# Optimization experiments

Measured on AMD Instinct MI355X. Metric: run time of the kernel, lower is better.

The kernel has to match this reference:

```python
import jax, jax.numpy as jnp
import numpy as np


def setup_inputs() -> dict:
    key = jax.random.key(0)
    ks = jax.random.split(key, 20)
    B, T, E, U, D, O = 64, 2048, 256, 256, 256, 32000
    s = lambda k, shp, fan: (jax.random.normal(k, shp, jnp.float32) * (1.0 / np.sqrt(fan)))
    return {
        'inputs': jax.random.normal(ks[0], (B, D), jnp.float32),
        'stm': jax.random.normal(ks[1], (B, U), jnp.float32),
        'x_seq': jax.random.normal(ks[2], (B, T, E), jnp.float32),
        'V_a': s(ks[3], (U + E,), U + E),
        'W_a': s(ks[4], (U + E, U + E), U + E),
        'W_r': s(ks[5], (D, U), D), 'U_r': s(ks[6], (U, U), U), 'C_r': s(ks[7], (E, U), E), 'b_r': jnp.zeros((U,), jnp.float32),
        'W_z': s(ks[8], (D, U), D), 'U_z': s(ks[9], (U, U), U), 'C_z': s(ks[10], (E, U), E), 'b_z': jnp.zeros((U,), jnp.float32),
        'W_p': s(ks[11], (D, U), D), 'U_p': s(ks[12], (U, U), U), 'C_p': s(ks[13], (E, U), E), 'b_p': jnp.zeros((U,), jnp.float32),
        'W_o': s(ks[14], (D, O), D), 'U_o': s(ks[15], (U, O), U), 'C_o': s(ks[16], (E, O), E), 'b_o': jnp.zeros((O,), jnp.float32),
    }


def reference(inputs, stm, x_seq, V_a, W_a,
              W_r, U_r, C_r, b_r,
              W_z, U_z, C_z, b_z,
              W_p, U_p, C_p, b_p,
              W_o, U_o, C_o, b_o):
    B, T, E = x_seq.shape
    U = stm.shape[-1]
    # Bahdanau additive attention: concat repeated state with encoder seq
    _stm = jnp.broadcast_to(stm[:, None, :], (B, T, U))          # [B,T,U]
    cat = jnp.concatenate([_stm, x_seq], axis=-1)                 # [B,T,U+E]
    et = jnp.einsum('btc,c->bt', jnp.tanh(jnp.einsum('btc,cd->btd', cat, W_a)), V_a)
    at = jax.nn.softmax(et, axis=1)                               # exp / sum over T
    context = jnp.einsum('bt,bte->be', at, x_seq)                 # [B,E]
    # GRU-style gates conditioned on input, previous state, and context
    rt = jax.nn.sigmoid(inputs @ W_r + stm @ U_r + context @ C_r + b_r)
    zt = jax.nn.sigmoid(inputs @ W_z + stm @ U_z + context @ C_z + b_z)
    s_tp = jnp.tanh(inputs @ W_p + (rt * stm) @ U_p + context @ C_p + b_p)
    st = (1.0 - zt) * stm + zt * s_tp                             # new state [B,U]
    output = jax.nn.softmax(inputs @ W_o + stm @ U_o + context @ C_o + b_o, axis=-1)  # [B,O]
    return output, st
```

## Files before the change

### kernel.cpp

```cpp
#include <hip/hip_runtime.h>
#include <hip/hip_bf16.h>

#define B_ 64
#define T_ 2048
#define E_ 256
#define U_ 256
#define O_ 32000
#define UE_ 512

typedef __attribute__((ext_vector_type(8))) short bf16x8;
typedef __attribute__((ext_vector_type(4))) float f32x4;

__device__ __forceinline__ unsigned short f2bf(float f){
  __hip_bfloat16 h = __float2bfloat16(f);
  return __builtin_bit_cast(unsigned short, h);
}
__device__ __forceinline__ unsigned pk2bf(float a, float b){
  return (unsigned)f2bf(a) | ((unsigned)f2bf(b) << 16);
}
__device__ __forceinline__ bf16x8 pack8(const float* v0, const float* v1){
  float4 x = *(const float4*)v0;
  float4 y = *(const float4*)v1;
  uint4 pk;
  pk.x = pk2bf(x.x, x.y); pk.y = pk2bf(x.z, x.w);
  pk.z = pk2bf(y.x, y.y); pk.w = pk2bf(y.z, y.w);
  return __builtin_bit_cast(bf16x8, pk);
}
__device__ __forceinline__ float ftanh(float x){
  float e = __expf(2.0f*x);
  return 1.0f - 2.0f/(e + 1.0f);
}
__device__ __forceinline__ float fsig(float x){
  return 1.0f/(1.0f + __expf(-x));
}

__global__ __launch_bounds__(256)
void prep_kernel(const float* __restrict__ Wa, const float* __restrict__ stm,
                 unsigned short* __restrict__ bpack, float* __restrict__ sp){
  if (blockIdx.x < 64){
    int idx = blockIdx.x*256 + threadIdx.x;
    int n = idx & 511;
    int ktg = idx >> 9;
    int erow = ktg * 8;
    unsigned short o[8];
#pragma unroll
    for (int i = 0; i < 8; ++i)
      o[i] = f2bf(Wa[(256 + erow + i)*512 + n]);
    uint4 v;
    v.x = (unsigned)o[0] | ((unsigned)o[1] << 16);
    v.y = (unsigned)o[2] | ((unsigned)o[3] << 16);
    v.z = (unsigned)o[4] | ((unsigned)o[5] << 16);
    v.w = (unsigned)o[6] | ((unsigned)o[7] << 16);
    ((uint4*)bpack)[idx] = v;
  } else {
    int tid = threadIdx.x;
    int w = tid >> 6, l = tid & 63, c = l & 15, g = l >> 4;
    int n0 = (blockIdx.x - 64)*64 + w*16;
    f32x4 zero = {0.f,0.f,0.f,0.f};
    f32x4 acc[4];
#pragma unroll
    for (int mt = 0; mt < 4; ++mt) acc[mt] = zero;
#pragma unroll
    for (int ks = 0; ks < 8; ++ks){
      int kg = ks*32 + 8*g;
      bf16x8 a[4];
#pragma unroll
      for (int mt = 0; mt < 4; ++mt){
        const float* ap = stm + (mt*16 + c)*256 + kg;
        a[mt] = pack8(ap, ap + 4);
      }
      const float* bpt = Wa + (size_t)kg*512 + n0 + c;
      float bv[8];
#pragma unroll
      for (int i = 0; i < 8; ++i) bv[i] = bpt[(size_t)i*512];
      uint4 pk;
      pk.x = pk2bf(bv[0], bv[1]); pk.y = pk2bf(bv[2], bv[3]);
      pk.z = pk2bf(bv[4], bv[5]); pk.w = pk2bf(bv[6], bv[7]);
      bf16x8 bfr = __builtin_bit_cast(bf16x8, pk);
#pragma unroll
      for (int mt = 0; mt < 4; ++mt)
        acc[mt] = __builtin_amdgcn_mfma_f32_16x16x32_bf16(a[mt], bfr, acc[mt], 0, 0, 0);
    }
#pragma unroll
    for (int mt = 0; mt < 4; ++mt)
#pragma unroll
      for (int r = 0; r < 4; ++r){
        int m = mt*16 + 4*g + r;
        sp[m*512 + n0 + c] = acc[mt][r];
      }
  }
}

__global__ __launch_bounds__(512, 4)
void et_flash_kernel(const float* __restrict__ xseq, const unsigned short* __restrict__ bpack,
                     const float* __restrict__ va, const float* __restrict__ sp,
                     float* __restrict__ msbuf, float* __restrict__ uctxp){
  __shared__ __align__(16) uint4 sA4[2048];
  __shared__ float sVa[512];
  __shared__ float sSp[512];
  __shared__ float sEt[8][64];
  __shared__ float sE[64];
  int tid = threadIdx.x;
  int w = tid >> 6, l = tid & 63, c = l & 15, g = l >> 4;
  int m0 = blockIdx.x * 64;
  int b  = m0 >> 11;

  const float4* x4 = (const float4*)xseq + (size_t)m0 * 64;
  uint2* sA2 = (uint2*)sA4;
#pragma unroll
  for (int i = 0; i < 8; ++i){
    int p = i*512 + tid;
    int row = p >> 6, kq = p & 63;
    float4 v = x4[row*64 + kq];
    uint2 u;
    u.x = pk2bf(v.x, v.y);
    u.y = pk2bf(v.z, v.w);
    int s = ((row>>4)*8 + (kq>>3))*64 + ((kq>>1)&3)*16 + (row&15);
    sA2[(s ^ ((s>>4)&7))*2 + (kq&1)] = u;
  }
  sVa[tid] = va[tid];
  sSp[tid] = sp[b*512 + tid];
  __syncthreads();

  f32x4 zero = {0.f, 0.f, 0.f, 0.f};
  f32x4 acc[4][4];
#pragma unroll
  for (int mt = 0; mt < 4; ++mt)
#pragma unroll
    for (int tc = 0; tc < 4; ++tc) acc[mt][tc] = zero;

  const bf16x8* bp = (const bf16x8*)bpack;
#pragma unroll
  for (int ks = 0; ks < 8; ++ks){
    bf16x8 aw[4], bx[4];
    int bbase = (ks*4 + g)*512 + w*64 + c;
#pragma unroll
    for (int mt = 0; mt < 4; ++mt)
      aw[mt] = bp[bbase + mt*16];
#pragma unroll
    for (int tc = 0; tc < 4; ++tc){
      int idx = (tc*8 + ks)*64 + l;
      bx[tc] = *(const bf16x8*)&sA4[idx ^ ((idx>>4)&7)];
    }
    __builtin_amdgcn_s_setprio(1);
#pragma unroll
    for (int mt = 0; mt < 4; ++mt)
#pragma unroll
      for (int tc = 0; tc < 4; ++tc)
        acc[mt][tc] = __builtin_amdgcn_mfma_f32_16x16x32_bf16(aw[mt], bx[tc], acc[mt][tc], 0, 0, 0);
    __builtin_amdgcn_s_setprio(0);
  }

  float p[4] = {0.f, 0.f, 0.f, 0.f};
#pragma unroll
  for (int mt = 0; mt < 4; ++mt){
    int nb = w*64 + mt*16 + 4*g;
    float4 vav = *(const float4*)&sVa[nb];
    float4 spv = *(const float4*)&sSp[nb];
#pragma unroll
    for (int tc = 0; tc < 4; ++tc){
#pragma unroll
      for (int r = 0; r < 4; ++r){
        float vv = acc[mt][tc][r] + ((const float*)&spv)[r];
        p[tc] += ((const float*)&vav)[r] * ftanh(vv);
      }
    }
  }
#pragma unroll
  for (int tc = 0; tc < 4; ++tc){
    p[tc] += __shfl_xor(p[tc], 16, 64);
    p[tc] += __shfl_xor(p[tc], 32, 64);
  }
  if (l < 16){
#pragma unroll
    for (int tc = 0; tc < 4; ++tc)
      sEt[w][tc*16 + c] = p[tc];
  }
  __syncthreads();

  if (tid < 64){
    float e = 0.f;
#pragma unroll
    for (int ww = 0; ww < 8; ++ww) e += sEt[ww][tid];
    float m = e;
#pragma unroll
    for (int off = 1; off < 64; off <<= 1) m = fmaxf(m, __shfl_xor(m, off, 64));
    float ex = __expf(e - m);
    float s = ex;
#pragma unroll
    for (int off = 1; off < 64; off <<= 1) s += __shfl_xor(s, off, 64);
    sE[tid] = ex;
    if (tid == 0){
      msbuf[blockIdx.x*2]     = m;
      msbuf[blockIdx.x*2 + 1] = s;
    }
  }
  __syncthreads();

  {
    int e = tid & 255, th = tid >> 8;
    int ks = e >> 5, gg = (e >> 3) & 3, ii = e & 7;
    const unsigned short* sU = (const unsigned short*)sA4;
    float a0 = 0.f;
#pragma unroll
    for (int tt = 0; tt < 32; ++tt){
      int t = th*32 + tt;
      int mt = t >> 4, cc = t & 15;
      int slt = (mt*8 + ks)*64 + gg*16 + cc;
      unsigned short hv = sU[(size_t)(slt ^ ((slt>>4)&7))*8 + ii];
      float xv = __builtin_bit_cast(float, ((unsigned)hv) << 16);
      a0 += sE[t] * xv;
    }
    uctxp[((size_t)blockIdx.x*2 + th)*256 + e] = a0;
  }
}

__global__ void ctx_x1_kernel(const float* __restrict__ msbuf, const float* __restrict__ uctxp,
                              const float* __restrict__ inputs, const float* __restrict__ stm,
                              unsigned short* __restrict__ X1bf){
  int b = blockIdx.x, e = threadIdx.x;
  float M = -INFINITY;
#pragma unroll 4
  for (int j = 0; j < 32; ++j) M = fmaxf(M, msbuf[(32*b + j)*2]);
  float S = 0.f;
  float acc = 0.f;
#pragma unroll 4
  for (int j = 0; j < 32; ++j){
    float wj = __expf(msbuf[(32*b + j)*2] - M);
    S += msbuf[(32*b + j)*2 + 1] * wj;
    size_t base = ((size_t)(32*b + j)*2)*256 + e;
    acc += (uctxp[base] + uctxp[base + 256]) * wj;
  }
  float ctx = acc / S;
  X1bf[b*768 + e]        = f2bf(inputs[b*256 + e]);
  X1bf[b*768 + 256 + e]  = f2bf(stm[b*256 + e]);
  X1bf[b*768 + 512 + e]  = f2bf(ctx);
}

__global__ __launch_bounds__(256)
void gates1_kernel(const unsigned short* __restrict__ X1bf, const float* __restrict__ stm,
                   const float* __restrict__ Wr, const float* __restrict__ Ur,
                   const float* __restrict__ Cr, const float* __restrict__ brr,
                   const float* __restrict__ Wz, const float* __restrict__ Uz,
                   const float* __restrict__ Cz, const float* __restrict__ bzz,
                   const float* __restrict__ Wp, const float* __restrict__ Cp,
                   const float* __restrict__ bpp,
                   float* __restrict__ rs, float* __restrict__ ztb, float* __restrict__ pic){
  int tid = threadIdx.x;
  int w = tid >> 6, l = tid & 63, c = l & 15, g = l >> 4;
  int n0 = blockIdx.x*64 + w*16;
  int gate = n0 >> 8;
  int col0 = n0 & 255;
  const float* W0; const float* W1; const float* W2; const float* bias;
  if (gate == 0){ W0 = Wr; W1 = Ur; W2 = Cr; bias = brr; }
  else if (gate == 1){ W0 = Wz; W1 = Uz; W2 = Cz; bias = bzz; }
  else { W0 = Wp; W1 = nullptr; W2 = Cp; bias = bpp; }

  f32x4 zero = {0.f,0.f,0.f,0.f};
  f32x4 acc[4];
#pragma unroll
  for (int mt = 0; mt < 4; ++mt) acc[mt] = zero;

#pragma unroll
  for (int ph = 0; ph < 3; ++ph){
    const float* src = (ph == 0) ? W0 : (ph == 1) ? W1 : W2;
    if (src == nullptr) continue;
#pragma unroll
    for (int ks = 0; ks < 8; ++ks){
      int kg = ks*32 + 8*g;
      bf16x8 a[4];
#pragma unroll
      for (int mt = 0; mt < 4; ++mt)
        a[mt] = *(const bf16x8*)&X1bf[(mt*16 + c)*768 + ph*256 + kg];
      const float* bpt = src + (size_t)kg*256 + col0 + c;
      float bv[8];
#pragma unroll
      for (int i = 0; i < 8; ++i) bv[i] = bpt[(size_t)i*256];
      uint4 pk;
      pk.x = pk2bf(bv[0], bv[1]); pk.y = pk2bf(bv[2], bv[3]);
      pk.z = pk2bf(bv[4], bv[5]); pk.w = pk2bf(bv[6], bv[7]);
      bf16x8 bfr = __builtin_bit_cast(bf16x8, pk);
#pragma unroll
      for (int mt = 0; mt < 4; ++mt)
        acc[mt] = __builtin_amdgcn_mfma_f32_16x16x32_bf16(a[mt], bfr, acc[mt], 0, 0, 0);
    }
  }

  int n = col0 + c;
  float bi = bias[n];
#pragma unroll
  for (int mt = 0; mt < 4; ++mt)
#pragma unroll
    for (int r = 0; r < 4; ++r){
      int m = mt*16 + 4*g + r;
      float pre = acc[mt][r] + bi;
      if (gate == 0)      rs[m*256 + n]  = fsig(pre) * stm[m*256 + n];
      else if (gate == 1) ztb[m*256 + n] = fsig(pre);
      else                pic[m*256 + n] = pre;
    }
}

__global__ __launch_bounds__(256)
void gates2_kernel(const float* __restrict__ rs, const float* __restrict__ Up,
                   const float* __restrict__ pic, const float* __restrict__ ztb,
                   const float* __restrict__ stm, float* __restrict__ stout){
  int tid = threadIdx.x;
  int w = tid >> 6, l = tid & 63, c = l & 15, g = l >> 4;
  int n0 = blockIdx.x*64 + w*16;
  f32x4 zero = {0.f,0.f,0.f,0.f};
  f32x4 acc[4];
#pragma unroll
  for (int mt = 0; mt < 4; ++mt) acc[mt] = zero;
#pragma unroll
  for (int ks = 0; ks < 8; ++ks){
    int kg = ks*32 + 8*g;
    bf16x8 a[4];
#pragma unroll
    for (int mt = 0; mt < 4; ++mt){
      const float* ap = rs + (mt*16 + c)*256 + kg;
      a[mt] = pack8(ap, ap + 4);
    }
    const float* bpt = Up + (size_t)kg*256 + n0 + c;
    float bv[8];
#pragma unroll
    for (int i = 0; i < 8; ++i) bv[i] = bpt[(size_t)i*256];
    uint4 pk;
    pk.x = pk2bf(bv[0], bv[1]); pk.y = pk2bf(bv[2], bv[3]);
    pk.z = pk2bf(bv[4], bv[5]); pk.w = pk2bf(bv[6], bv[7]);
    bf16x8 bfr = __builtin_bit_cast(bf16x8, pk);
#pragma unroll
    for (int mt = 0; mt < 4; ++mt)
      acc[mt] = __builtin_amdgcn_mfma_f32_16x16x32_bf16(a[mt], bfr, acc[mt], 0, 0, 0);
  }
#pragma unroll
  for (int mt = 0; mt < 4; ++mt)
#pragma unroll
    for (int r = 0; r < 4; ++r){
      int m = mt*16 + 4*g + r;
      int o = m*256 + n0 + c;
      float ap = pic[o] + acc[mt][r];
      float z = ztb[o];
      stout[o] = (1.f - z)*stm[o] + z*ftanh(ap);
    }
}

__global__ __launch_bounds__(512)
void logits_mfma_kernel(const unsigned short* __restrict__ X1bf,
                        const float* __restrict__ Wo, const float* __restrict__ Uo,
                        const float* __restrict__ Co, const float* __restrict__ boo,
                        float* __restrict__ outl, float* __restrict__ part2){
  __shared__ float sAcc[16][4][64];
  __shared__ float sMx[4][64];
  __shared__ float sSx[4][64];
  int tid = threadIdx.x;
  int w = tid >> 6, l = tid & 63, c = l & 15, g = l >> 4;
  int wc = w & 3;
  int kh = w >> 2;
  int n0 = blockIdx.x*64 + wc*16;
  f32x4 zero = {0.f,0.f,0.f,0.f};
  f32x4 acc[4];
#pragma unroll
  for (int mt = 0; mt < 4; ++mt) acc[mt] = zero;

#pragma unroll
  for (int ph = 0; ph < 3; ++ph){
    const float* src = (ph == 0) ? Wo : (ph == 1) ? Uo : Co;
#pragma unroll
    for (int kss = 0; kss < 4; ++kss){
      int ks = 2*kss + kh;
      int kg = ph*256 + ks*32 + 8*g;
      bf16x8 a[4];
#pragma unroll
      for (int mt = 0; mt < 4; ++mt)
        a[mt] = *(const bf16x8*)&X1bf[(mt*16 + c)*768 + kg];
      const float* bpt = src + (size_t)(ks*32 + 8*g)*32000 + n0 + c;
      float bv[8];
#pragma unroll
      for (int i = 0; i < 8; ++i) bv[i] = bpt[(size_t)i*32000];
      uint4 pk;
      pk.x = pk2bf(bv[0], bv[1]);
      pk.y = pk2bf(bv[2], bv[3]);
      pk.z = pk2bf(bv[4], bv[5]);
      pk.w = pk2bf(bv[6], bv[7]);
      bf16x8 bfr = __builtin_bit_cast(bf16x8, pk);
#pragma unroll
      for (int mt = 0; mt < 4; ++mt)
        acc[mt] = __builtin_amdgcn_mfma_f32_16x16x32_bf16(a[mt], bfr, acc[mt], 0, 0, 0);
    }
  }

  if (kh == 1){
#pragma unroll
    for (int mt = 0; mt < 4; ++mt)
#pragma unroll
      for (int r = 0; r < 4; ++r)
        sAcc[mt*4 + r][wc][l] = acc[mt][r];
  }
  __syncthreads();

  bool active = (kh == 0);
  float vv[4][4];
  if (active){
    float bias = boo[n0 + c];
#pragma unroll
    for (int mt = 0; mt < 4; ++mt)
#pragma unroll
      for (int r = 0; r < 4; ++r){
        int m = mt*16 + 4*g + r;
        vv[mt][r] = acc[mt][r] + sAcc[mt*4 + r][wc][l] + bias;
        outl[(size_t)m*32000 + n0 + c] = vv[mt][r];
      }
    float mx[4][4];
#pragma unroll
    for (int mt = 0; mt < 4; ++mt)
#pragma unroll
      for (int r = 0; r < 4; ++r) mx[mt][r] = vv[mt][r];
#pragma unroll
    for (int mask = 1; mask < 16; mask <<= 1)
#pragma unroll
      for (int mt = 0; mt < 4; ++mt)
#pragma unroll
        for (int r = 0; r < 4; ++r)
          mx[mt][r] = fmaxf(mx[mt][r], __shfl_xor(mx[mt][r], mask, 64));
    if (c == 0)
#pragma unroll
      for (int mt = 0; mt < 4; ++mt)
#pragma unroll
        for (int r = 0; r < 4; ++r)
          sMx[wc][mt*16 + 4*g + r] = mx[mt][r];
  }
  __syncthreads();
  if (active){
    float sx[4][4];
#pragma unroll
    for (int mt = 0; mt < 4; ++mt)
#pragma unroll
      for (int r = 0; r < 4; ++r){
        int row = mt*16 + 4*g + r;
        float M = fmaxf(fmaxf(sMx[0][row], sMx[1][row]), fmaxf(sMx[2][row], sMx[3][row]));
        sx[mt][r] = __expf(vv[mt][r] - M);
      }
#pragma unroll
    for (int mask = 1; mask < 16; mask <<= 1)
#pragma unroll
      for (int mt = 0; mt < 4; ++mt)
#pragma unroll
        for (int r = 0; r < 4; ++r)
          sx[mt][r] += __shfl_xor(sx[mt][r], mask, 64);
    if (c == 0)
#pragma unroll
      for (int mt = 0; mt < 4; ++mt)
#pragma unroll
        for (int r = 0; r < 4; ++r)
          sSx[wc][mt*16 + 4*g + r] = sx[mt][r];
  }
  __syncthreads();
  if (tid < 64){
    int row = tid;
    float M = fmaxf(fmaxf(sMx[0][row], sMx[1][row]), fmaxf(sMx[2][row], sMx[3][row]));
    float S = sSx[0][row] + sSx[1][row] + sSx[2][row] + sSx[3][row];
    part2[((size_t)blockIdx.x*64 + row)*2]     = M;
    part2[((size_t)blockIdx.x*64 + row)*2 + 1] = S;
  }
}

__global__ void sm_comb_kernel(const float* __restrict__ part2, float* __restrict__ fin){
  __shared__ float red[8];
  __shared__ float red2[8];
  int b = blockIdx.x;
  int tid = threadIdx.x;
  float M = -INFINITY, S = 0.f;
  if (tid < 500){
    M = part2[((size_t)tid*64 + b)*2];
    S = part2[((size_t)tid*64 + b)*2 + 1];
  }
  float m1 = M;
#pragma unroll
  for (int off = 1; off < 64; off <<= 1) m1 = fmaxf(m1, __shfl_xor(m1, off, 64));
  int wv = tid >> 6;
  if ((tid & 63) == 0) red[wv] = m1;
  __syncthreads();
  float Mg = red[0];
#pragma unroll
  for (int i = 1; i < 8; ++i) Mg = fmaxf(Mg, red[i]);
  float s1 = (tid < 500) ? S * __expf(M - Mg) : 0.f;
#pragma unroll
  for (int off = 1; off < 64; off <<= 1) s1 += __shfl_xor(s1, off, 64);
  if ((tid & 63) == 0) red2[wv] = s1;
  __syncthreads();
  if (tid == 0){
    float St = 0.f;
#pragma unroll
    for (int i = 0; i < 8; ++i) St += red2[i];
    fin[b*2] = Mg;
    fin[b*2 + 1] = St;
  }
}

__global__ void sm_norm_kernel(float* __restrict__ logits, const float* __restrict__ fin){
  int bid = blockIdx.x;
  int b = bid >> 3, ch = bid & 7;
  int base = b*32000 + ch*4000;
  int tid = threadIdx.x;
  float M = fin[2*b];
  float inv = 1.0f / fin[2*b + 1];
#pragma unroll
  for (int i = 0; i < 16; ++i){
    int idx = i*256 + tid;
    if (idx < 4000){
      int o = base + idx;
      logits[o] = __expf(logits[o] - M) * inv;
    }
  }
}

extern "C" void kernel_launch(void* const* d_in, const int* in_sizes, int n_in,
                              void* d_out, int out_size, void* d_ws, size_t ws_size,
                              hipStream_t stream) {
  const float* inputs = (const float*)d_in[0];
  const float* stm    = (const float*)d_in[1];
  const float* xseq   = (const float*)d_in[2];
  const float* Va     = (const float*)d_in[3];
  const float* Wa     = (const float*)d_in[4];
  const float* Wr = (const float*)d_in[5];
  const float* Ur = (const float*)d_in[6];
  const float* Cr = (const float*)d_in[7];
  const float* br = (const float*)d_in[8];
  const float* Wz = (const float*)d_in[9];
  const float* Uz = (const float*)d_in[10];
  const float* Cz = (const float*)d_in[11];
  const float* bz = (const float*)d_in[12];
  const float* Wp = (const float*)d_in[13];
  const float* Up = (const float*)d_in[14];
  const float* Cp = (const float*)d_in[15];
  const float* bp = (const float*)d_in[16];
  const float* Wo = (const float*)d_in[17];
  const float* Uo = (const float*)d_in[18];
  const float* Co = (const float*)d_in[19];
  const float* bo = (const float*)d_in[20];

  float* out   = (float*)d_out;
  float* stout = out + (size_t)B_*O_;

  float* wsf = (float*)d_ws;
  unsigned short* bpack = (unsigned short*)d_ws;
  float* sp    = wsf + 65536;
  float* msbuf = wsf + 98304;
  float* uctxp = wsf + 102400;
  float* fin   = wsf + 98304;
  float* part2 = wsf + 102400;
  unsigned short* X1bf = (unsigned short*)(wsf + 1150976);
  float* rs    = wsf + 1176576;
  float* ztb   = wsf + 1192960;
  float* pic   = wsf + 1209344;

  prep_kernel<<<72, 256, 0, stream>>>(Wa, stm, bpack, sp);
  et_flash_kernel<<<2048, 512, 0, stream>>>(xseq, bpack, Va, sp, msbuf, uctxp);
  ctx_x1_kernel<<<64, 256, 0, stream>>>(msbuf, uctxp, inputs, stm, X1bf);
  gates1_kernel<<<12, 256, 0, stream>>>(X1bf, stm, Wr, Ur, Cr, br,
                                        Wz, Uz, Cz, bz, Wp, Cp, bp,
                                        rs, ztb, pic);
  gates2_kernel<<<4, 256, 0, stream>>>(rs, Up, pic, ztb, stm, stout);
  logits_mfma_kernel<<<500, 512, 0, stream>>>(X1bf, Wo, Uo, Co, bo, out, part2);
  sm_comb_kernel<<<64, 512, 0, stream>>>(part2, fin);
  sm_norm_kernel<<<512, 256, 0, stream>>>(out, fin);
}
```

Measured before the change: 162.3 us.

## Pre-pack output weights to bf16 inside attention kernel, consume in logits

The attention kernel gains a tail phase that converts the fp32 Wo/Uo/Co weights into a bf16 layout packed in groups of 8 k-values, written to workspace. The idea is to hide that conversion behind the memory-bound attention pass. A new logits kernel then reads the prepacked weights with one 16-byte load per lane, so the fp32 weight traffic and on-the-fly packing leave the logits stage. The path runs only when the workspace is large enough. It adds extra strided fp32 reads and a bf16 write to the attention kernel, and the packing is redone on every call.

```diff
diff --git a/kernel.cpp b/kernel.cpp
--- a/kernel.cpp
+++ b/kernel.cpp
@@ -94,7 +94,10 @@
 __global__ __launch_bounds__(512, 4)
 void et_flash_kernel(const float* __restrict__ xseq, const unsigned short* __restrict__ bpack,
                      const float* __restrict__ va, const float* __restrict__ sp,
-                     float* __restrict__ msbuf, float* __restrict__ uctxp){
+                     float* __restrict__ msbuf, float* __restrict__ uctxp,
+                     const float* __restrict__ Wo2, const float* __restrict__ Uo2,
+                     const float* __restrict__ Co2, unsigned short* __restrict__ wpack,
+                     int doconv){
   __shared__ __align__(16) uint4 sA4[2048];
   __shared__ float sVa[512];
   __shared__ float sSp[512];
@@ -212,6 +215,25 @@
       a0 += sE[t] * xv;
     }
     uctxp[((size_t)blockIdx.x*2 + th)*256 + e] = a0;
+  }
+
+  if (doconv){
+    for (int q0 = tid; q0 < 1500; q0 += 512){
+      int q = blockIdx.x*1500 + q0;
+      int o = q / 32000;
+      int n = q - o*32000;
+      int ph2 = o >> 5;
+      int rowk = (o & 31) * 8;
+      const float* srcw = (ph2 == 0) ? Wo2 : (ph2 == 1) ? Uo2 : Co2;
+      const float* pw = srcw + (size_t)rowk*32000 + n;
+      float wv0[8];
+#pragma unroll
+      for (int i = 0; i < 8; ++i) wv0[i] = pw[(size_t)i*32000];
+      uint4 pkw;
+      pkw.x = pk2bf(wv0[0], wv0[1]); pkw.y = pk2bf(wv0[2], wv0[3]);
+      pkw.z = pk2bf(wv0[4], wv0[5]); pkw.w = pk2bf(wv0[6], wv0[7]);
+      ((uint4*)wpack)[(size_t)o*32000 + n] = pkw;
+    }
   }
 }
 
@@ -342,6 +364,118 @@
       float z = ztb[o];
       stout[o] = (1.f - z)*stm[o] + z*ftanh(ap);
     }
+}
+
+__global__ __launch_bounds__(512)
+void logits_pk_kernel(const unsigned short* __restrict__ X1bf,
+                      const unsigned short* __restrict__ wpack,
+                      const float* __restrict__ boo,
+                      float* __restrict__ outl, float* __restrict__ part2){
+  __shared__ float sAcc[16][4][64];
+  __shared__ float sMx[4][64];
+  __shared__ float sSx[4][64];
+  int tid = threadIdx.x;
+  int w = tid >> 6, l = tid & 63, c = l & 15, g = l >> 4;
+  int wc = w & 3;
+  int kh = w >> 2;
+  int n0 = blockIdx.x*64 + wc*16;
+  const bf16x8* wp = (const bf16x8*)wpack;
+  f32x4 zero = {0.f,0.f,0.f,0.f};
+  f32x4 acc[4];
+#pragma unroll
+  for (int mt = 0; mt < 4; ++mt) acc[mt] = zero;
+
+#pragma unroll
+  for (int ph = 0; ph < 3; ++ph){
+#pragma unroll
+    for (int kss = 0; kss < 4; ++kss){
+      int ks = 2*kss + kh;
+      int kg = ph*256 + ks*32 + 8*g;
+      bf16x8 a[4];
+#pragma unroll
+      for (int mt = 0; mt < 4; ++mt)
+        a[mt] = *(const bf16x8*)&X1bf[(mt*16 + c)*768 + kg];
+      int o = (ph*8 + ks)*4 + g;
+      bf16x8 bfr = wp[(size_t)o*32000 + n0 + c];
+#pragma unroll
+      for (int mt = 0; mt < 4; ++mt)
+        acc[mt] = __builtin_amdgcn_mfma_f32_16x16x32_bf16(a[mt], bfr, acc[mt], 0, 0, 0);
+    }
+  }
+
+  if (kh == 1){
+#pragma unroll
+    for (int mt = 0; mt < 4; ++mt)
+#pragma unroll
+      for (int r = 0; r < 4; ++r)
+        sAcc[mt*4 + r][wc][l] = acc[mt][r];
+  }
+  __syncthreads();
+
+  bool active = (kh == 0);
+  float vv[4][4];
+  if (active){
+    float bias = boo[n0 + c];
+#pragma unroll
+    for (int mt = 0; mt < 4; ++mt)
+#pragma unroll
+      for (int r = 0; r < 4; ++r){
+        int m = mt*16 + 4*g + r;
+        vv[mt][r] = acc[mt][r] + sAcc[mt*4 + r][wc][l] + bias;
+        outl[(size_t)m*32000 + n0 + c] = vv[mt][r];
+      }
+    float mx[4][4];
+#pragma unroll
+    for (int mt = 0; mt < 4; ++mt)
+#pragma unroll
+      for (int r = 0; r < 4; ++r) mx[mt][r] = vv[mt][r];
+#pragma unroll
+    for (int mask = 1; mask < 16; mask <<= 1)
+#pragma unroll
+      for (int mt = 0; mt < 4; ++mt)
+#pragma unroll
+        for (int r = 0; r < 4; ++r)
+          mx[mt][r] = fmaxf(mx[mt][r], __shfl_xor(mx[mt][r], mask, 64));
+    if (c == 0)
+#pragma unroll
+      for (int mt = 0; mt < 4; ++mt)
+#pragma unroll
+        for (int r = 0; r < 4; ++r)
+          sMx[wc][mt*16 + 4*g + r] = mx[mt][r];
+  }
+  __syncthreads();
+  if (active){
+    float sx[4][4];
+#pragma unroll
+    for (int mt = 0; mt < 4; ++mt)
+#pragma unroll
+      for (int r = 0; r < 4; ++r){
+        int row = mt*16 + 4*g + r;
+        float M = fmaxf(fmaxf(sMx[0][row], sMx[1][row]), fmaxf(sMx[2][row], sMx[3][row]));
+        sx[mt][r] = __expf(vv[mt][r] - M);
+      }
+#pragma unroll
+    for (int mask = 1; mask < 16; mask <<= 1)
+#pragma unroll
+      for (int mt = 0; mt < 4; ++mt)
+#pragma unroll
+        for (int r = 0; r < 4; ++r)
+          sx[mt][r] += __shfl_xor(sx[mt][r], mask, 64);
+    if (c == 0)
+#pragma unroll
+      for (int mt = 0; mt < 4; ++mt)
+#pragma unroll
+        for (int r = 0; r < 4; ++r)
+          sSx[wc][mt*16 + 4*g + r] = sx[mt][r];
+  }
+  __syncthreads();
+  if (tid < 64){
+    int row = tid;
+    float M = fmaxf(fmaxf(sMx[0][row], sMx[1][row]), fmaxf(sMx[2][row], sMx[3][row]));
+    float S = sSx[0][row] + sSx[1][row] + sSx[2][row] + sSx[3][row];
+    part2[((size_t)blockIdx.x*64 + row)*2]     = M;
+    part2[((size_t)blockIdx.x*64 + row)*2 + 1] = S;
+  }
 }
 
 __global__ __launch_bounds__(512)
@@ -553,15 +687,21 @@
   float* rs    = wsf + 1176576;
   float* ztb   = wsf + 1192960;
   float* pic   = wsf + 1209344;
+  unsigned short* wpack = (unsigned short*)(wsf + 1225728);
+  int big = (ws_size >= (size_t)54054912) ? 1 : 0;
 
   prep_kernel<<<72, 256, 0, stream>>>(Wa, stm, bpack, sp);
-  et_flash_kernel<<<2048, 512, 0, stream>>>(xseq, bpack, Va, sp, msbuf, uctxp);
+  et_flash_kernel<<<2048, 512, 0, stream>>>(xseq, bpack, Va, sp, msbuf, uctxp,
+                                            Wo, Uo, Co, wpack, big);
   ctx_x1_kernel<<<64, 256, 0, stream>>>(msbuf, uctxp, inputs, stm, X1bf);
   gates1_kernel<<<12, 256, 0, stream>>>(X1bf, stm, Wr, Ur, Cr, br,
                                         Wz, Uz, Cz, bz, Wp, Cp, bp,
                                         rs, ztb, pic);
   gates2_kernel<<<4, 256, 0, stream>>>(rs, Up, pic, ztb, stm, stout);
-  logits_mfma_kernel<<<500, 512, 0, stream>>>(X1bf, Wo, Uo, Co, bo, out, part2);
+  if (big)
+    logits_pk_kernel<<<500, 512, 0, stream>>>(X1bf, wpack, bo, out, part2);
+  else
+    logits_mfma_kernel<<<500, 512, 0, stream>>>(X1bf, Wo, Uo, Co, bo, out, part2);
   sm_comb_kernel<<<64, 512, 0, stream>>>(part2, fin);
   sm_norm_kernel<<<512, 256, 0, stream>>>(out, fin);
 }
```

Result: slower. 184.8 us (+13.9%).
